# Performance work log

Hardware: AMD Instinct MI355X
Metric: run time of the kernel (lower is better)

The kernel has to match this reference:

```python
import jax, jax.numpy as jnp
import numpy as np

B = 2097152  # batch (rows the original Python loop iterated over)
D = 64       # feature dim == label/one-hot width (ret = zeros_like(xs))


def setup_inputs() -> dict:
    key = jax.random.key(0)
    k1, k2, k3 = jax.random.split(key, 3)
    x = jax.random.normal(k1, (B, D), dtype=jnp.float32)
    # Enclave dense-layer parameters (opaque in the original; materialized here).
    W = jax.random.normal(k2, (D, D), dtype=jnp.float32) * (1.0 / np.sqrt(D))
    b = jax.random.normal(k3, (D,), dtype=jnp.float32) * 0.01
    return {"x": x, "W": W, "b": b}


def reference(x, W, b):
    # Batched replacement for the per-sample Python loop:
    #   label_i = enclave_dense(x_i)  ->  argmax(x_i @ W + b)
    #   ret[i, label_i] = 1           ->  one_hot over width D (= zeros_like(x))
    logits = x @ W + b                      # [B, D]
    labels = jnp.argmax(logits, axis=-1)    # [B]
    return jax.nn.one_hot(labels, x.shape[-1], dtype=x.dtype)  # [B, D]
```

## Files before the change

kernel.cpp:

```cpp
#include <hip/hip_runtime.h>


typedef __attribute__((ext_vector_type(2))) float f32x2;
typedef __attribute__((ext_vector_type(4))) float f32x4;

#define W2(WR, P) (*(const f32x2*)((WR) + ((P) << 1)))

#define PK1(C, XKK, WR, P) (C) = __builtin_elementwise_fma((XKK), W2((WR), (P)), (C));

#define PK32(XK, WR) {                                                        \
    const f32x2 xkk_ = {(XK), (XK)};                                          \
    PK1(c0,  xkk_, (WR), 0)  PK1(c1,  xkk_, (WR), 1)                          \
    PK1(c2,  xkk_, (WR), 2)  PK1(c3,  xkk_, (WR), 3)                          \
    PK1(c4,  xkk_, (WR), 4)  PK1(c5,  xkk_, (WR), 5)                          \
    PK1(c6,  xkk_, (WR), 6)  PK1(c7,  xkk_, (WR), 7)                          \
    PK1(c8,  xkk_, (WR), 8)  PK1(c9,  xkk_, (WR), 9)                          \
    PK1(c10, xkk_, (WR), 10) PK1(c11, xkk_, (WR), 11)                         \
    PK1(c12, xkk_, (WR), 12) PK1(c13, xkk_, (WR), 13)                         \
    PK1(c14, xkk_, (WR), 14) PK1(c15, xkk_, (WR), 15)                         \
    PK1(c16, xkk_, (WR), 16) PK1(c17, xkk_, (WR), 17)                         \
    PK1(c18, xkk_, (WR), 18) PK1(c19, xkk_, (WR), 19)                         \
    PK1(c20, xkk_, (WR), 20) PK1(c21, xkk_, (WR), 21)                         \
    PK1(c22, xkk_, (WR), 22) PK1(c23, xkk_, (WR), 23)                         \
    PK1(c24, xkk_, (WR), 24) PK1(c25, xkk_, (WR), 25)                         \
    PK1(c26, xkk_, (WR), 26) PK1(c27, xkk_, (WR), 27)                         \
    PK1(c28, xkk_, (WR), 28) PK1(c29, xkk_, (WR), 29)                         \
    PK1(c30, xkk_, (WR), 30) PK1(c31, xkk_, (WR), 31)                         \
}

#define PKBLK(XV, KK)                                                         \
    PK32((XV).x, W + (KK) * 256)                                              \
    PK32((XV).y, W + (KK) * 256 + 64)                                         \
    PK32((XV).z, W + (KK) * 256 + 128)                                        \
    PK32((XV).w, W + (KK) * 256 + 192)

#define ADDB2(C, P) (C) += *(const f32x2*)(bp + ((P) << 1));

#define CHK(V, J)                                                             \
    if ((V) > best) { best = (V); idx = (J); }

#define CHK2(C, P) CHK((C).x, 2 * (P)) CHK((C).y, 2 * (P) + 1)

__global__ __launch_bounds__(256) void onehot_argmax_kernel(
    const float* __restrict__ x, const float* __restrict__ W,
    const float* __restrict__ b, float* __restrict__ out, int nrows)
{
    const int lane = threadIdx.x & 63;
    const int wave = threadIdx.x >> 6;
    const long waveRow0 = (long)blockIdx.x * 256 + (long)wave * 64;
    long r = waveRow0 + lane;
    if (r >= nrows) r = nrows - 1;

    const f32x2 z2 = {0.f, 0.f};
    f32x2 c0 = z2,  c1 = z2,  c2 = z2,  c3 = z2,  c4 = z2,  c5 = z2,  c6 = z2,  c7 = z2;
    f32x2 c8 = z2,  c9 = z2,  c10 = z2, c11 = z2, c12 = z2, c13 = z2, c14 = z2, c15 = z2;
    f32x2 c16 = z2, c17 = z2, c18 = z2, c19 = z2, c20 = z2, c21 = z2, c22 = z2, c23 = z2;
    f32x2 c24 = z2, c25 = z2, c26 = z2, c27 = z2, c28 = z2, c29 = z2, c30 = z2, c31 = z2;

    const f32x4* __restrict__ xr4 = (const f32x4*)(x + r * 64);
    const f32x4 x0 = xr4[0],  x1 = xr4[1],  x2 = xr4[2],  x3 = xr4[3];
    const f32x4 x4 = xr4[4],  x5 = xr4[5],  x6 = xr4[6],  x7 = xr4[7];
    const f32x4 x8 = xr4[8],  x9 = xr4[9],  x10 = xr4[10], x11 = xr4[11];
    const f32x4 x12 = xr4[12], x13 = xr4[13], x14 = xr4[14], x15 = xr4[15];

    PKBLK(x0, 0)   PKBLK(x1, 1)   PKBLK(x2, 2)   PKBLK(x3, 3)
    PKBLK(x4, 4)   PKBLK(x5, 5)   PKBLK(x6, 6)   PKBLK(x7, 7)
    PKBLK(x8, 8)   PKBLK(x9, 9)   PKBLK(x10, 10) PKBLK(x11, 11)
    PKBLK(x12, 12) PKBLK(x13, 13) PKBLK(x14, 14) PKBLK(x15, 15)

    const float* __restrict__ bp = b;
    ADDB2(c0, 0)   ADDB2(c1, 1)   ADDB2(c2, 2)   ADDB2(c3, 3)
    ADDB2(c4, 4)   ADDB2(c5, 5)   ADDB2(c6, 6)   ADDB2(c7, 7)
    ADDB2(c8, 8)   ADDB2(c9, 9)   ADDB2(c10, 10) ADDB2(c11, 11)
    ADDB2(c12, 12) ADDB2(c13, 13) ADDB2(c14, 14) ADDB2(c15, 15)
    ADDB2(c16, 16) ADDB2(c17, 17) ADDB2(c18, 18) ADDB2(c19, 19)
    ADDB2(c20, 20) ADDB2(c21, 21) ADDB2(c22, 22) ADDB2(c23, 23)
    ADDB2(c24, 24) ADDB2(c25, 25) ADDB2(c26, 26) ADDB2(c27, 27)
    ADDB2(c28, 28) ADDB2(c29, 29) ADDB2(c30, 30) ADDB2(c31, 31)

    float best = c0.x;
    int idx = 0;
    CHK(c0.y, 1)
    CHK2(c1, 1)   CHK2(c2, 2)   CHK2(c3, 3)   CHK2(c4, 4)
    CHK2(c5, 5)   CHK2(c6, 6)   CHK2(c7, 7)   CHK2(c8, 8)
    CHK2(c9, 9)   CHK2(c10, 10) CHK2(c11, 11) CHK2(c12, 12)
    CHK2(c13, 13) CHK2(c14, 14) CHK2(c15, 15) CHK2(c16, 16)
    CHK2(c17, 17) CHK2(c18, 18) CHK2(c19, 19) CHK2(c20, 20)
    CHK2(c21, 21) CHK2(c22, 22) CHK2(c23, 23) CHK2(c24, 24)
    CHK2(c25, 25) CHK2(c26, 26) CHK2(c27, 27) CHK2(c28, 28)
    CHK2(c29, 29) CHK2(c30, 30) CHK2(c31, 31)

    float4* __restrict__ outw = (float4*)(out + waveRow0 * 64);
    const long remf4 = ((long)nrows - waveRow0) * 16;
#pragma unroll
    for (int i = 0; i < 16; ++i) {
        const int f = i * 64 + lane;
        const int idx_r = __shfl(idx, f >> 4, 64);
        const bool m = ((idx_r >> 2) == (f & 15));
        const int c = idx_r & 3;
        float4 v;
        v.x = (m && c == 0) ? 1.0f : 0.0f;
        v.y = (m && c == 1) ? 1.0f : 0.0f;
        v.z = (m && c == 2) ? 1.0f : 0.0f;
        v.w = (m && c == 3) ? 1.0f : 0.0f;
        if (f < remf4) outw[f] = v;
    }
}

extern "C" void kernel_launch(void* const* d_in, const int* in_sizes, int n_in,
                              void* d_out, int out_size, void* d_ws, size_t ws_size,
                              hipStream_t stream) {
    const float* x = (const float*)d_in[0];
    const float* W = (const float*)d_in[1];
    const float* b = (const float*)d_in[2];
    float* out = (float*)d_out;

    const int nrows = in_sizes[0] / 64;
    dim3 block(256);
    dim3 grid((nrows + 255) / 256);
    hipLaunchKernelGGL(onehot_argmax_kernel, grid, block, 0, stream,
                       x, W, b, out, nrows);
}
```

Baseline: 936.7 us.

## Stage x tiles into LDS with coalesced direct global-to-LDS loads and XOR swizzle

Each wave now copies its 64-row by 64-float tile of x into shared memory with buffer-style global_load_lds instructions, laid out so consecutive lanes read consecutive 16-byte chunks. The tile is stored with an XOR swizzle so each lane can then read its own row from LDS without bank conflicts. This replaces the earlier per-lane strided row loads, which touched 256-byte-separated addresses per lane and coalesced poorly. It costs 64 KB of LDS per block, which limits occupancy (the launch bounds now request two blocks per CU), and adds a full vmcnt wait before compute.

```diff
diff --git a/kernel.cpp b/kernel.cpp
--- a/kernel.cpp
+++ b/kernel.cpp
@@ -41,27 +41,60 @@
 
 #define CHK2(C, P) CHK((C).x, 2 * (P)) CHK((C).y, 2 * (P) + 1)
 
-__global__ __launch_bounds__(256) void onehot_argmax_kernel(
+#define SWZ_SRC(I) (((I) & ~15) | (((I) & 15) ^ (((I) >> 4) & 7)))
+
+__global__ __launch_bounds__(256, 2) void onehot_argmax_kernel(
     const float* __restrict__ x, const float* __restrict__ W,
     const float* __restrict__ b, float* __restrict__ out, int nrows)
 {
     const int lane = threadIdx.x & 63;
     const int wave = threadIdx.x >> 6;
     const long waveRow0 = (long)blockIdx.x * 256 + (long)wave * 64;
-    long r = waveRow0 + lane;
-    if (r >= nrows) r = nrows - 1;
+
+    __shared__ f32x4 sbuf[4][1024];
+    f32x4* __restrict__ wbuf = &sbuf[wave][0];
+
+    const float* __restrict__ tile = x + waveRow0 * 64;
+    const long remf4 = ((long)nrows - waveRow0) * 16;
+
+    if (remf4 >= 1024) {
+#pragma unroll
+        for (int t = 0; t < 16; ++t) {
+            const int I = t * 64 + lane;
+            const int f = SWZ_SRC(I);
+            __builtin_amdgcn_global_load_lds(
+                (const __attribute__((address_space(1))) void*)(tile + (long)f * 4),
+                (__attribute__((address_space(3))) void*)(wbuf + t * 64),
+                16, 0, 0);
+        }
+    } else {
+#pragma unroll
+        for (int t = 0; t < 16; ++t) {
+            const int I = t * 64 + lane;
+            const int f = SWZ_SRC(I);
+            if (f < remf4) {
+                __builtin_amdgcn_global_load_lds(
+                    (const __attribute__((address_space(1))) void*)(tile + (long)f * 4),
+                    (__attribute__((address_space(3))) void*)(wbuf + t * 64),
+                    16, 0, 0);
+            }
+        }
+    }
+    asm volatile("s_waitcnt vmcnt(0)" ::: "memory");
+
+    const int swz = lane & 7;
+    const int rb = lane << 4;
+#define LDX(Q) wbuf[rb | ((Q) ^ swz)]
+    const f32x4 x0 = LDX(0),  x1 = LDX(1),  x2 = LDX(2),  x3 = LDX(3);
+    const f32x4 x4 = LDX(4),  x5 = LDX(5),  x6 = LDX(6),  x7 = LDX(7);
+    const f32x4 x8 = LDX(8),  x9 = LDX(9),  x10 = LDX(10), x11 = LDX(11);
+    const f32x4 x12 = LDX(12), x13 = LDX(13), x14 = LDX(14), x15 = LDX(15);
 
     const f32x2 z2 = {0.f, 0.f};
     f32x2 c0 = z2,  c1 = z2,  c2 = z2,  c3 = z2,  c4 = z2,  c5 = z2,  c6 = z2,  c7 = z2;
     f32x2 c8 = z2,  c9 = z2,  c10 = z2, c11 = z2, c12 = z2, c13 = z2, c14 = z2, c15 = z2;
     f32x2 c16 = z2, c17 = z2, c18 = z2, c19 = z2, c20 = z2, c21 = z2, c22 = z2, c23 = z2;
     f32x2 c24 = z2, c25 = z2, c26 = z2, c27 = z2, c28 = z2, c29 = z2, c30 = z2, c31 = z2;
-
-    const f32x4* __restrict__ xr4 = (const f32x4*)(x + r * 64);
-    const f32x4 x0 = xr4[0],  x1 = xr4[1],  x2 = xr4[2],  x3 = xr4[3];
-    const f32x4 x4 = xr4[4],  x5 = xr4[5],  x6 = xr4[6],  x7 = xr4[7];
-    const f32x4 x8 = xr4[8],  x9 = xr4[9],  x10 = xr4[10], x11 = xr4[11];
-    const f32x4 x12 = xr4[12], x13 = xr4[13], x14 = xr4[14], x15 = xr4[15];
 
     PKBLK(x0, 0)   PKBLK(x1, 1)   PKBLK(x2, 2)   PKBLK(x3, 3)
     PKBLK(x4, 4)   PKBLK(x5, 5)   PKBLK(x6, 6)   PKBLK(x7, 7)
@@ -91,7 +124,6 @@
     CHK2(c29, 29) CHK2(c30, 30) CHK2(c31, 31)
 
     float4* __restrict__ outw = (float4*)(out + waveRow0 * 64);
-    const long remf4 = ((long)nrows - waveRow0) * 16;
 #pragma unroll
     for (int i = 0; i < 16; ++i) {
         const int f = i * 64 + lane;
```

Measured after the change: 934.7 us. Within noise of the previous version (-0.2%).
